# Kernel optimization log

Hardware: AMD Instinct MI355X
Metric: run time of the kernel (lower is better)

## Reference

```python
import jax, jax.numpy as jnp
import numpy as np

B, N, D, NS, HID = 256, 1024, 64, 8, 128
ITERS, SINK_ITERS, MESH_ITERS = 3, 8, 4
MESH_LR = 3.0
EPS = 1e-8


def _grid():
    # build_coords with latent_resolution=(32,32): meshgrid('xy'), flattened to [1024,2]
    x = np.linspace(0.0, 1.0, 32)
    xv, yv = np.meshgrid(x, x)
    g = np.stack([xv.reshape(-1), yv.reshape(-1)], axis=-1)
    return jnp.asarray(g, dtype=jnp.float32)


def layer_norm(x, g, b):
    m = jnp.mean(x, axis=-1, keepdims=True)
    v = jnp.var(x, axis=-1, keepdims=True)
    return (x - m) * jax.lax.rsqrt(v + 1e-5) * g + b


def cdist(k, q):
    # Euclidean pairwise distance: k [b,n,d], q [b,s,d] -> [b,n,s]
    d2 = (jnp.sum(k * k, -1)[..., :, None] + jnp.sum(q * q, -1)[..., None, :]
          - 2.0 * jnp.einsum('bnd,bsd->bns', k, q))
    return jnp.sqrt(jnp.maximum(d2, 1e-12))


def sinkhorn(C, a, b, u=None, v=None, n_iters=SINK_ITERS):
    # log-domain Sinkhorn; C [b,n,s], row marginal a [b,n], col marginal b [b,s]
    log_a = jnp.log(a + EPS)
    log_b = jnp.log(b + EPS)
    if u is None:
        u = jnp.zeros_like(a)
    if v is None:
        v = jnp.zeros_like(b)
    K = -C

    def body(carry, _):
        u, v = carry
        u = log_a - jax.scipy.special.logsumexp(K + v[..., None, :], axis=-1)
        v = log_b - jax.scipy.special.logsumexp(K + u[..., :, None], axis=-2)
        return (u, v), None

    (u, v), _ = jax.lax.scan(body, (u, v), None, length=n_iters)
    P = jnp.exp(K + u[..., :, None] + v[..., None, :])
    return P, u, v


def minimize_entropy_of_sinkhorn(C0, a, b, mesh_lr=MESH_LR, n_mesh_iters=MESH_ITERS):
    # MESH: gradient descent on the cost matrix to minimize Sinkhorn plan entropy
    def ent(C):
        P, u, v = sinkhorn(C, a, b)
        H = -jnp.sum(P * jnp.log(P + EPS))
        return H, (u, v)

    C = C0
    u = v = None
    for _ in range(n_mesh_iters):
        (_, (u, v)), g = jax.value_and_grad(ent, has_aux=True)(C)
        C = C - mesh_lr * g
    return C, u, v


def gru_cell(x, h, w_ih, w_hh, b_ih, b_hh):
    gi = x @ w_ih.T + b_ih
    gh = h @ w_hh.T + b_hh
    i_r, i_z, i_n = jnp.split(gi, 3, axis=-1)
    h_r, h_z, h_n = jnp.split(gh, 3, axis=-1)
    r = jax.nn.sigmoid(i_r + h_r)
    z = jax.nn.sigmoid(i_z + h_z)
    n = jnp.tanh(i_n + r * h_n)
    return (1.0 - z) * n + z * h


def setup_inputs() -> dict:
    key = jax.random.key(0)
    ks = jax.random.split(key, 16)
    s = D ** -0.5
    inp = {
        'inputs': jax.random.normal(ks[0], (B, N, D), jnp.float32),
        'noise': jax.random.normal(ks[1], (B, NS, D), jnp.float32),
        'slots_mu': jax.random.normal(ks[2], (1, 1, D), jnp.float32),
        'slots_sigma': jax.random.uniform(ks[3], (1, 1, D), jnp.float32),
        'Wq': jax.random.normal(ks[4], (D, D), jnp.float32) * s,
        'Wk': jax.random.normal(ks[5], (D, D), jnp.float32) * s,
        'Wv': jax.random.normal(ks[6], (D, D), jnp.float32) * s,
        'gru_w_ih': jax.random.normal(ks[7], (3 * D, D), jnp.float32) * s,
        'gru_w_hh': jax.random.normal(ks[8], (3 * D, D), jnp.float32) * s,
        'gru_b_ih': jnp.zeros((3 * D,), jnp.float32),
        'gru_b_hh': jnp.zeros((3 * D,), jnp.float32),
        'fc1_w': jax.random.normal(ks[9], (HID, D), jnp.float32) * s,
        'fc1_b': jnp.zeros((HID,), jnp.float32),
        'fc2_w': jax.random.normal(ks[10], (D, HID), jnp.float32) * (HID ** -0.5),
        'fc2_b': jnp.zeros((D,), jnp.float32),
        'ln_in_g': jnp.ones((D,), jnp.float32), 'ln_in_b': jnp.zeros((D,), jnp.float32),
        'ln_slots_g': jnp.ones((D,), jnp.float32), 'ln_slots_b': jnp.zeros((D,), jnp.float32),
        'ln_ff_g': jnp.ones((D,), jnp.float32), 'ln_ff_b': jnp.zeros((D,), jnp.float32),
        'wi_w': jax.random.normal(ks[11], (1, D), jnp.float32) * s,
        'wi_b': jnp.zeros((1,), jnp.float32),
        'ws_w': jax.random.normal(ks[12], (1, D), jnp.float32) * s,
        'ws_b': jnp.zeros((1,), jnp.float32),
    }
    return inp


def _forward(inputs, noise, slots_mu, slots_sigma, Wq, Wk, Wv,
             gru_w_ih, gru_w_hh, gru_b_ih, gru_b_hh,
             fc1_w, fc1_b, fc2_w, fc2_b,
             ln_in_g, ln_in_b, ln_slots_g, ln_slots_b, ln_ff_g, ln_ff_b,
             wi_w, wi_b, ws_w, ws_b):
    b_s, n, d = inputs.shape
    n_s = NS
    # slots ~ Normal(mu, |sigma|+eps) via reparameterized noise
    slots = slots_mu + (jnp.abs(slots_sigma) + EPS) * noise  # [b, n_s, d]

    x = layer_norm(inputs, ln_in_g, ln_in_b)
    k = x @ Wk.T
    v = x @ Wv.T
    grid = _grid()  # [N, 2]
    a = jax.nn.softmax((x @ wi_w.T + wi_b)[..., 0], axis=-1) * n_s  # [b, n]

    for _ in range(ITERS):
        slots_prev = slots
        s_n = layer_norm(slots, ln_slots_g, ln_slots_b)
        bm = jax.nn.softmax((s_n @ ws_w.T + ws_b)[..., 0], axis=-1) * n_s  # [b, n_s]
        q = s_n @ Wq.T
        C = cdist(k, q)  # [b, n, n_s]
        C, p, qq = minimize_entropy_of_sinkhorn(C, a, bm)
        attn, _, _ = sinkhorn(C, a, bm, u=p, v=qq)
        attn = jnp.transpose(attn, (0, 2, 1))  # [b, n_s, n]
        updates = attn @ v  # [b, n_s, d]
        slot_pos = jnp.einsum('bqk,kd->bqd', attn, grid)  # [b, n_s, 2]
        slots = gru_cell(updates.reshape(b_s * n_s, d),
                         slots_prev.reshape(b_s * n_s, d),
                         gru_w_ih, gru_w_hh, gru_b_ih, gru_b_hh).reshape(b_s, n_s, d)
        slots = slots + (jax.nn.relu(layer_norm(slots, ln_ff_g, ln_ff_b) @ fc1_w.T + fc1_b) @ fc2_w.T + fc2_b)
    return slots, slot_pos.reshape(b_s, n_s, 2), attn


def reference(inputs, noise, slots_mu, slots_sigma, Wq, Wk, Wv,
              gru_w_ih, gru_w_hh, gru_b_ih, gru_b_hh,
              fc1_w, fc1_b, fc2_w, fc2_b,
              ln_in_g, ln_in_b, ln_slots_g, ln_slots_b, ln_ff_g, ln_ff_b,
              wi_w, wi_b, ws_w, ws_b):
    return _forward(inputs, noise, slots_mu, slots_sigma, Wq, Wk, Wv,
                    gru_w_ih, gru_w_hh, gru_b_ih, gru_b_hh,
                    fc1_w, fc1_b, fc2_w, fc2_b,
                    ln_in_g, ln_in_b, ln_slots_g, ln_slots_b, ln_ff_g, ln_ff_b,
                    wi_w, wi_b, ws_w, ws_b)
```

## Files before the change

kernel.cpp:

```cpp
#include <hip/hip_runtime.h>
#include <math.h>

#define NB   256
#define NN   1024
#define ND   64
#define NSL  8
#define NHID 128
#define N_SINK 8
#define N_MESH 4
#define F_LR  3.0f
#define F_EPS 1e-8f

__global__ __launch_bounds__(256) void k_pre(
    const float* __restrict__ inp, const float* __restrict__ Wk,
    const float* __restrict__ lng, const float* __restrict__ lnb,
    const float* __restrict__ wiw, const float* __restrict__ wib,
    float* __restrict__ xout, float* __restrict__ kkout, float* __restrict__ wilog) {
  __shared__ __align__(16) float xs[4][64];
  int wv = threadIdx.x >> 6, ln = threadIdx.x & 63;
  size_t row = (size_t)blockIdx.x * 4 + wv;
  float xi = inp[row * 64 + ln];
  float s1 = xi, s2 = xi * xi;
  #pragma unroll
  for (int m = 32; m >= 1; m >>= 1) { s1 += __shfl_xor(s1, m, 64); s2 += __shfl_xor(s2, m, 64); }
  float mean = s1 * (1.f / 64.f);
  float var  = s2 * (1.f / 64.f) - mean * mean;
  float xn = (xi - mean) * rsqrtf(var + 1e-5f) * lng[ln] + lnb[ln];
  xs[wv][ln] = xn;
  xout[row * 64 + ln] = xn;
  float wl = xn * wiw[ln];
  #pragma unroll
  for (int m = 32; m >= 1; m >>= 1) wl += __shfl_xor(wl, m, 64);
  __syncthreads();
  const float4* w4 = (const float4*)(Wk + ln * 64);
  const float4* x4 = (const float4*)xs[wv];
  float ko = 0.f;
  #pragma unroll
  for (int c = 0; c < 16; ++c) {
    float4 a = w4[c], xv = x4[c];
    ko += a.x * xv.x + a.y * xv.y + a.z * xv.z + a.w * xv.w;
  }
  float kk = ko * ko;
  #pragma unroll
  for (int m = 32; m >= 1; m >>= 1) kk += __shfl_xor(kk, m, 64);
  if (ln == 0) { kkout[row] = kk; wilog[row] = wl + wib[0]; }
}

__global__ __launch_bounds__(1024) void k_mega(
    const float* __restrict__ noise, const float* __restrict__ mu,
    const float* __restrict__ sigma,
    const float* __restrict__ xg, const float* __restrict__ kkg,
    const float* __restrict__ wilogg,
    const float* __restrict__ Wq, const float* __restrict__ Wk,
    const float* __restrict__ Wv,
    const float* __restrict__ wih, const float* __restrict__ whh,
    const float* __restrict__ bih, const float* __restrict__ bhh,
    const float* __restrict__ fc1w, const float* __restrict__ fc1b,
    const float* __restrict__ fc2w, const float* __restrict__ fc2b,
    const float* __restrict__ lns_g, const float* __restrict__ lns_b,
    const float* __restrict__ lnf_g, const float* __restrict__ lnf_b,
    const float* __restrict__ wsw, const float* __restrict__ wsb,
    float* __restrict__ out_slots, float* __restrict__ out_pos,
    float* __restrict__ out_attn) {
  __shared__ __align__(16) float know[8][NN];
  __shared__ __align__(16) union {
    float fhist[N_SINK][NN];
    float part[16][8][64];
  } U;
  __shared__ __align__(16) float dsb[NN];
  __shared__ __align__(16) float slot_lds[8][64];
  __shared__ __align__(16) float sn[8][64];
  __shared__ __align__(16) float qsh[8][64];
  __shared__ __align__(16) float qs[8][64];
  __shared__ __align__(16) float updl[8][64];
  __shared__ __align__(16) float ys[8][64];
  __shared__ __align__(16) float rs[8][128];
  __shared__ float gbc[8];
  __shared__ float vbarbc[8];
  __shared__ float ghist[N_SINK][8];
  __shared__ float gBh[N_SINK][8];
  __shared__ float bmv[8], q2s[8], Bs[8], rBs[8];
  __shared__ float redf[16], bcf[1];

  int b = blockIdx.x, tid = threadIdx.x;
  int wv = tid >> 6, ln = tid & 63;

  if (tid < 512) {
    slot_lds[tid >> 6][ln] = mu[ln] + (fabsf(sigma[ln]) + F_EPS) * noise[(size_t)b * 512 + tid];
  }
  float wl = wilogg[(size_t)b * NN + tid];
  float m0 = wl;
  #pragma unroll
  for (int s = 32; s >= 1; s >>= 1) m0 = fmaxf(m0, __shfl_xor(m0, s, 64));
  if (ln == 0) redf[wv] = m0;
  __syncthreads();
  if (tid == 0) { float a = redf[0]; for (int w = 1; w < 16; ++w) a = fmaxf(a, redf[w]); bcf[0] = a; }
  __syncthreads();
  m0 = bcf[0];
  float e0 = __expf(wl - m0), se0 = e0;
  #pragma unroll
  for (int s = 32; s >= 1; s >>= 1) se0 += __shfl_xor(se0, s, 64);
  __syncthreads();
  if (ln == 0) redf[wv] = se0;
  __syncthreads();
  if (tid == 0) { float a = 0.f; for (int w = 0; w < 16; ++w) a += redf[w]; bcf[0] = a; }
  __syncthreads();
  float Ai  = 8.f * e0 / bcf[0] + F_EPS;
  float rAi = __frcp_rn(Ai);
  float kk = kkg[(size_t)b * NN + tid];
  const float4* xrow4 = (const float4*)(xg + ((size_t)b * NN + tid) * ND);

  for (int it = 0; it < 3; ++it) {
    if (wv < 8) {
      float x = slot_lds[wv][ln];
      float s1 = x, s2 = x * x;
      #pragma unroll
      for (int m = 32; m >= 1; m >>= 1) { s1 += __shfl_xor(s1, m, 64); s2 += __shfl_xor(s2, m, 64); }
      float mean = s1 * (1.f / 64.f);
      float var  = s2 * (1.f / 64.f) - mean * mean;
      float xn = (x - mean) * rsqrtf(var + 1e-5f) * lns_g[ln] + lns_b[ln];
      sn[wv][ln] = xn;
      float wlg = xn * wsw[ln];
      #pragma unroll
      for (int m = 32; m >= 1; m >>= 1) wlg += __shfl_xor(wlg, m, 64);
      if (ln == 0) bmv[wv] = wlg + wsb[0];
    }
    __syncthreads();
    if (wv < 8) {
      const float4* w4 = (const float4*)(Wq + ln * 64);
      const float4* x4 = (const float4*)sn[wv];
      float q = 0.f;
      #pragma unroll
      for (int c = 0; c < 16; ++c) {
        float4 a = w4[c], xv = x4[c];
        q += a.x * xv.x + a.y * xv.y + a.z * xv.z + a.w * xv.w;
      }
      qsh[wv][ln] = q;
      float q2 = q * q;
      #pragma unroll
      for (int m = 32; m >= 1; m >>= 1) q2 += __shfl_xor(q2, m, 64);
      if (ln == 0) q2s[wv] = q2;
    }
    if (tid >= 512 && tid < 520) {
      int j = tid - 512;
      float mx = bmv[0];
      #pragma unroll
      for (int jj = 1; jj < 8; ++jj) mx = fmaxf(mx, bmv[jj]);
      float ss = 0.f;
      #pragma unroll
      for (int jj = 0; jj < 8; ++jj) ss += __expf(bmv[jj] - mx);
      float Bj = 8.f * __expf(bmv[j] - mx) / ss + F_EPS;
      Bs[j] = Bj; rBs[j] = __frcp_rn(Bj);
    }
    __syncthreads();
    if (wv < 8) {
      float qt = 0.f;
      for (int o = 0; o < 64; ++o) qt = fmaf(qsh[wv][o], Wk[o * 64 + ln], qt);
      qs[wv][ln] = qt;
    }
    __syncthreads();

    float Mreg[8];
    {
      float dot[8];
      #pragma unroll
      for (int j = 0; j < 8; ++j) dot[j] = 0.f;
      #pragma unroll 4
      for (int c = 0; c < 16; ++c) {
        float4 xv = xrow4[c];
        #pragma unroll
        for (int j = 0; j < 8; ++j) {
          const float4 qv = *(const float4*)&qs[j][c * 4];
          dot[j] += xv.x * qv.x + xv.y * qv.y + xv.z * qv.z + xv.w * qv.w;
        }
      }
      #pragma unroll
      for (int j = 0; j < 8; ++j) {
        float d2 = kk + q2s[j] - 2.f * dot[j];
        float K = -sqrtf(fmaxf(d2, 1e-12f));
        Mreg[j] = __expf(K);
        know[j][tid] = Mreg[j];
      }
    }
    float f = 0.f;
    for (int phase = 0; phase <= N_MESH; ++phase) {
      bool cold = (phase < N_MESH);
      for (int t = 0; t < N_SINK; ++t) {
        float se = 0.f;
        if (cold && t == 0) {
          #pragma unroll
          for (int j = 0; j < 8; ++j) se += Mreg[j];
        } else {
          #pragma unroll
          for (int j = 0; j < 8; ++j) se += Mreg[j] * gbc[j];
        }
        f = __fdividef(Ai, se);
        U.fhist[t][tid] = f;
        __syncthreads();
        if (wv < 8) {
          float S = 0.f;
          #pragma unroll
          for (int k = 0; k < 16; ++k) {
            int i = ln + k * 64;
            S += know[wv][i] * U.fhist[t][i];
          }
          #pragma unroll
          for (int d = 32; d >= 1; d >>= 1) S += __shfl_xor(S, d, 64);
          if (ln == 0) {
            float g = __fdividef(Bs[wv], S);
            gbc[wv] = g; ghist[t][wv] = g; gBh[t][wv] = g * rBs[wv];
          }
        }
        __syncthreads();
      }
      if (phase == N_MESH) break;

      float Kbar[8], ubarT;
      {
        float gsum = 0.f;
        #pragma unroll
        for (int j = 0; j < 8; ++j) {
          float P  = Mreg[j] * f * gbc[j];
          float pe = P + F_EPS;
          float gp = -(__logf(pe) + __fdividef(P, pe)) * P;
          Kbar[j] = gp; gsum += gp;
        }
        ubarT = gsum;
      }
      if (wv < 8) {
        float gw = gbc[wv];
        float S = 0.f;
        #pragma unroll
        for (int k = 0; k < 16; ++k) {
          int i = ln + k * 64;
          float P  = know[wv][i] * U.fhist[N_SINK - 1][i] * gw;
          float pe = P + F_EPS;
          S += -(__logf(pe) + __fdividef(P, pe)) * P;
        }
        #pragma unroll
        for (int d = 32; d >= 1; d >>= 1) S += __shfl_xor(S, d, 64);
        if (ln == 0) vbarbc[wv] = S;
      }
      __syncthreads();
      for (int t = N_SINK - 1; t >= 0; --t) {
        float ft = U.fhist[t][tid];
        float dsum = (t == N_SINK - 1) ? ubarT : 0.f;
        #pragma unroll
        for (int j = 0; j < 8; ++j) {
          float vw = vbarbc[j] * gBh[t][j] * (Mreg[j] * ft);
          Kbar[j] -= vw; dsum -= vw;
        }
        float dfa = dsum * ft * rAi;
        if (t > 0) {
          #pragma unroll
          for (int j = 0; j < 8; ++j) Kbar[j] -= dfa * Mreg[j] * ghist[t - 1][j];
          dsb[tid] = dfa;
          __syncthreads();
          if (wv < 8) {
            float S = 0.f;
            #pragma unroll
            for (int k = 0; k < 16; ++k) {
              int i = ln + k * 64;
              S += know[wv][i] * dsb[i];
            }
            #pragma unroll
            for (int d = 32; d >= 1; d >>= 1) S += __shfl_xor(S, d, 64);
            if (ln == 0) vbarbc[wv] = -ghist[t - 1][wv] * S;
          }
          __syncthreads();
        } else {
          #pragma unroll
          for (int j = 0; j < 8; ++j) Kbar[j] -= dfa * Mreg[j];
        }
      }
      #pragma unroll
      for (int j = 0; j < 8; ++j) {
        Mreg[j] *= __expf(-F_LR * Kbar[j]);
        know[j][tid] = Mreg[j];
      }
    }
    #pragma unroll
    for (int j = 0; j < 8; ++j) {
      float P = Mreg[j] * f * gbc[j];
      know[j][tid] = P;
      if (it == 2) out_attn[((size_t)b * 8 + j) * NN + tid] = P;
    }
    __syncthreads();

    {
      float acc[8];
      #pragma unroll
      for (int j = 0; j < 8; ++j) acc[j] = 0.f;
      const float* xc = xg + ((size_t)b * NN + wv * 64) * ND + ln;
      #pragma unroll 2
      for (int i0 = 0; i0 < 64; i0 += 4) {
        float x0 = xc[(size_t)(i0 + 0) * 64];
        float x1 = xc[(size_t)(i0 + 1) * 64];
        float x2 = xc[(size_t)(i0 + 2) * 64];
        float x3 = xc[(size_t)(i0 + 3) * 64];
        int ir = wv * 64 + i0;
        #pragma unroll
        for (int j = 0; j < 8; ++j) {
          float4 a = *(const float4*)&know[j][ir];
          acc[j] += a.x * x0 + a.y * x1 + a.z * x2 + a.w * x3;
        }
      }
      #pragma unroll
      for (int j = 0; j < 8; ++j) U.part[wv][j][ln] = acc[j];
    }
    if (it == 2 && wv < 8) {
      float px = 0.f, py = 0.f;
      #pragma unroll
      for (int k = 0; k < 16; ++k) {
        int i = ln + k * 64;
        float a = know[wv][i];
        px += a * (float)(i & 31);
        py += a * (float)(i >> 5);
      }
      #pragma unroll
      for (int m = 32; m >= 1; m >>= 1) { px += __shfl_xor(px, m, 64); py += __shfl_xor(py, m, 64); }
      if (ln == 0) {
        out_pos[(b * 8 + wv) * 2 + 0] = px * (1.f / 31.f);
        out_pos[(b * 8 + wv) * 2 + 1] = py * (1.f / 31.f);
      }
    }
    __syncthreads();
    if (wv < 8) {
      float s = 0.f;
      #pragma unroll
      for (int w = 0; w < 16; ++w) s += U.part[w][wv][ln];
      updl[wv][ln] = s;
    }
    __syncthreads();
    if (wv < 8) {
      const float4* w4 = (const float4*)(Wv + ln * 64);
      const float4* u4 = (const float4*)updl[wv];
      float updv = 0.f;
      #pragma unroll
      for (int c = 0; c < 16; ++c) {
        float4 uv = u4[c], wvv = w4[c];
        updv += uv.x * wvv.x + uv.y * wvv.y + uv.z * wvv.z + uv.w * wvv.w;
      }
      sn[wv][ln] = updv;
    }
    __syncthreads();

    float hn = 0.f;
    if (wv < 8) {
      float h = slot_lds[wv][ln];
      float gi0 = bih[ln], gi1 = bih[64 + ln], gi2 = bih[128 + ln];
      float gh0 = bhh[ln], gh1 = bhh[64 + ln], gh2 = bhh[128 + ln];
      const float4* x4 = (const float4*)sn[wv];
      const float4* h4 = (const float4*)slot_lds[wv];
      const float4* wi0 = (const float4*)(wih + (size_t)ln * 64);
      const float4* wi1 = (const float4*)(wih + (size_t)(64 + ln) * 64);
      const float4* wi2 = (const float4*)(wih + (size_t)(128 + ln) * 64);
      const float4* wh0 = (const float4*)(whh + (size_t)ln * 64);
      const float4* wh1 = (const float4*)(whh + (size_t)(64 + ln) * 64);
      const float4* wh2 = (const float4*)(whh + (size_t)(128 + ln) * 64);
      #pragma unroll 2
      for (int c = 0; c < 16; ++c) {
        float4 xv = x4[c], hv = h4[c], a;
        a = wi0[c]; gi0 += xv.x * a.x + xv.y * a.y + xv.z * a.z + xv.w * a.w;
        a = wi1[c]; gi1 += xv.x * a.x + xv.y * a.y + xv.z * a.z + xv.w * a.w;
        a = wi2[c]; gi2 += xv.x * a.x + xv.y * a.y + xv.z * a.z + xv.w * a.w;
        a = wh0[c]; gh0 += hv.x * a.x + hv.y * a.y + hv.z * a.z + hv.w * a.w;
        a = wh1[c]; gh1 += hv.x * a.x + hv.y * a.y + hv.z * a.z + hv.w * a.w;
        a = wh2[c]; gh2 += hv.x * a.x + hv.y * a.y + hv.z * a.z + hv.w * a.w;
      }
      float r = 1.f / (1.f + expf(-(gi0 + gh0)));
      float z = 1.f / (1.f + expf(-(gi1 + gh1)));
      float n = tanhf(gi2 + r * gh2);
      hn = (1.f - z) * n + z * h;
      float s1 = hn, s2 = hn * hn;
      #pragma unroll
      for (int m = 32; m >= 1; m >>= 1) { s1 += __shfl_xor(s1, m, 64); s2 += __shfl_xor(s2, m, 64); }
      float mean = s1 * (1.f / 64.f);
      float var  = s2 * (1.f / 64.f) - mean * mean;
      ys[wv][ln] = (hn - mean) * rsqrtf(var + 1e-5f) * lnf_g[ln] + lnf_b[ln];
    }
    __syncthreads();
    if (wv < 8) {
      float a0 = fc1b[ln], a1 = fc1b[64 + ln];
      const float4* y4 = (const float4*)ys[wv];
      const float4* f0 = (const float4*)(fc1w + (size_t)ln * 64);
      const float4* f1 = (const float4*)(fc1w + (size_t)(64 + ln) * 64);
      #pragma unroll 2
      for (int c = 0; c < 16; ++c) {
        float4 yv = y4[c], a = f0[c], bb = f1[c];
        a0 += yv.x * a.x + yv.y * a.y + yv.z * a.z + yv.w * a.w;
        a1 += yv.x * bb.x + yv.y * bb.y + yv.z * bb.z + yv.w * bb.w;
      }
      rs[wv][ln] = fmaxf(a0, 0.f);
      rs[wv][64 + ln] = fmaxf(a1, 0.f);
    }
    __syncthreads();
    if (wv < 8) {
      float o = fc2b[ln];
      const float4* r4 = (const float4*)rs[wv];
      const float4* f2 = (const float4*)(fc2w + (size_t)ln * 128);
      #pragma unroll 2
      for (int c = 0; c < 32; ++c) {
        float4 rv = r4[c], a = f2[c];
        o += rv.x * a.x + rv.y * a.y + rv.z * a.z + rv.w * a.w;
      }
      slot_lds[wv][ln] = hn + o;
    }
    __syncthreads();
  }
  if (tid < 512) out_slots[(size_t)b * 512 + tid] = slot_lds[tid >> 6][ln];
}

extern "C" void kernel_launch(void* const* d_in, const int* in_sizes, int n_in,
                              void* d_out, int out_size, void* d_ws, size_t ws_size,
                              hipStream_t stream) {
  const float* inputs = (const float*)d_in[0];
  const float* noise  = (const float*)d_in[1];
  const float* mu     = (const float*)d_in[2];
  const float* sigma  = (const float*)d_in[3];
  const float* Wq     = (const float*)d_in[4];
  const float* Wk     = (const float*)d_in[5];
  const float* Wv     = (const float*)d_in[6];
  const float* gwih   = (const float*)d_in[7];
  const float* gwhh   = (const float*)d_in[8];
  const float* gbih   = (const float*)d_in[9];
  const float* gbhh   = (const float*)d_in[10];
  const float* fc1w   = (const float*)d_in[11];
  const float* fc1b   = (const float*)d_in[12];
  const float* fc2w   = (const float*)d_in[13];
  const float* fc2b   = (const float*)d_in[14];
  const float* lnin_g = (const float*)d_in[15];
  const float* lnin_b = (const float*)d_in[16];
  const float* lns_g  = (const float*)d_in[17];
  const float* lns_b  = (const float*)d_in[18];
  const float* lnf_g  = (const float*)d_in[19];
  const float* lnf_b  = (const float*)d_in[20];
  const float* wi_w   = (const float*)d_in[21];
  const float* wi_b   = (const float*)d_in[22];
  const float* ws_w   = (const float*)d_in[23];
  const float* ws_b   = (const float*)d_in[24];

  float* out       = (float*)d_out;
  float* out_slots = out;
  float* out_pos   = out + NB * NSL * ND;
  float* out_attn  = out_pos + NB * NSL * 2;

  float* p = (float*)d_ws;
  float* xbuf  = p; p += (size_t)NB * NN * ND;
  float* kkbuf = p; p += (size_t)NB * NN;
  float* wilog = p; p += (size_t)NB * NN;

  k_pre<<<(NB * NN) / 4, 256, 0, stream>>>(inputs, Wk, lnin_g, lnin_b, wi_w, wi_b,
                                           xbuf, kkbuf, wilog);
  k_mega<<<NB, 1024, 0, stream>>>(noise, mu, sigma, xbuf, kkbuf, wilog,
                                  Wq, Wk, Wv, gwih, gwhh, gbih, gbhh,
                                  fc1w, fc1b, fc2w, fc2b,
                                  lns_g, lns_b, lnf_g, lnf_b, ws_w, ws_b,
                                  out_slots, out_pos, out_attn);
}
```

Before: 1.109 ms.

## Replace LDS column reductions with register wave reductions and fewer barriers

```diff
diff --git a/kernel.cpp b/kernel.cpp
--- a/kernel.cpp
+++ b/kernel.cpp
@@ -44,6 +44,14 @@
   #pragma unroll
   for (int m = 32; m >= 1; m >>= 1) kk += __shfl_xor(kk, m, 64);
   if (ln == 0) { kkout[row] = kk; wilog[row] = wl + wib[0]; }
+}
+
+__device__ __forceinline__ void wave_sum8(float* a) {
+  #pragma unroll
+  for (int m = 32; m >= 1; m >>= 1) {
+    #pragma unroll
+    for (int j = 0; j < 8; ++j) a[j] += __shfl_xor(a[j], m, 64);
+  }
 }
 
 __global__ __launch_bounds__(1024) void k_mega(
@@ -67,7 +75,7 @@
     float fhist[N_SINK][NN];
     float part[16][8][64];
   } U;
-  __shared__ __align__(16) float dsb[NN];
+  __shared__ __align__(16) float part8[2][16][8];
   __shared__ __align__(16) float slot_lds[8][64];
   __shared__ __align__(16) float sn[8][64];
   __shared__ __align__(16) float qsh[8][64];
@@ -75,8 +83,6 @@
   __shared__ __align__(16) float updl[8][64];
   __shared__ __align__(16) float ys[8][64];
   __shared__ __align__(16) float rs[8][128];
-  __shared__ float gbc[8];
-  __shared__ float vbarbc[8];
   __shared__ float ghist[N_SINK][8];
   __shared__ float gBh[N_SINK][8];
   __shared__ float bmv[8], q2s[8], Bs[8], rBs[8];
@@ -160,6 +166,8 @@
     }
     __syncthreads();
 
+    float Bsr = 0.f, rBsr = 0.f;
+    if (ln < 8) { Bsr = Bs[ln]; rBsr = rBs[ln]; }
     float Mreg[8];
     {
       float dot[8];
@@ -177,12 +185,10 @@
       #pragma unroll
       for (int j = 0; j < 8; ++j) {
         float d2 = kk + q2s[j] - 2.f * dot[j];
-        float K = -sqrtf(fmaxf(d2, 1e-12f));
-        Mreg[j] = __expf(K);
-        know[j][tid] = Mreg[j];
-      }
-    }
-    float f = 0.f;
+        Mreg[j] = __expf(-sqrtf(fmaxf(d2, 1e-12f)));
+      }
+    }
+    float f = 0.f, g[8];
     for (int phase = 0; phase <= N_MESH; ++phase) {
       bool cold = (phase < N_MESH);
       for (int t = 0; t < N_SINK; ++t) {
@@ -192,96 +198,102 @@
           for (int j = 0; j < 8; ++j) se += Mreg[j];
         } else {
           #pragma unroll
-          for (int j = 0; j < 8; ++j) se += Mreg[j] * gbc[j];
+          for (int j = 0; j < 8; ++j) se += Mreg[j] * g[j];
         }
         f = __fdividef(Ai, se);
         U.fhist[t][tid] = f;
+        float pp[8];
+        #pragma unroll
+        for (int j = 0; j < 8; ++j) pp[j] = Mreg[j] * f;
+        wave_sum8(pp);
+        if (ln == 0) {
+          #pragma unroll
+          for (int j = 0; j < 8; ++j) part8[t & 1][wv][j] = pp[j];
+        }
         __syncthreads();
-        if (wv < 8) {
+        float gv = 0.f;
+        if (ln < 8) {
           float S = 0.f;
           #pragma unroll
-          for (int k = 0; k < 16; ++k) {
-            int i = ln + k * 64;
-            S += know[wv][i] * U.fhist[t][i];
-          }
-          #pragma unroll
-          for (int d = 32; d >= 1; d >>= 1) S += __shfl_xor(S, d, 64);
-          if (ln == 0) {
-            float g = __fdividef(Bs[wv], S);
-            gbc[wv] = g; ghist[t][wv] = g; gBh[t][wv] = g * rBs[wv];
-          }
-        }
-        __syncthreads();
+          for (int w = 0; w < 16; ++w) S += part8[t & 1][w][ln];
+          gv = __fdividef(Bsr, S);
+          if (wv == 0) { ghist[t][ln] = gv; gBh[t][ln] = gv * rBsr; }
+        }
+        #pragma unroll
+        for (int j = 0; j < 8; ++j) g[j] = __shfl(gv, j, 64);
       }
       if (phase == N_MESH) break;
 
-      float Kbar[8], ubarT;
+      float Kbar[8], vbar[8], ubarT;
       {
-        float gsum = 0.f;
+        float pp[8], gsum = 0.f;
         #pragma unroll
         for (int j = 0; j < 8; ++j) {
-          float P  = Mreg[j] * f * gbc[j];
+          float P  = Mreg[j] * f * g[j];
           float pe = P + F_EPS;
           float gp = -(__logf(pe) + __fdividef(P, pe)) * P;
-          Kbar[j] = gp; gsum += gp;
+          Kbar[j] = gp; gsum += gp; pp[j] = gp;
         }
         ubarT = gsum;
-      }
-      if (wv < 8) {
-        float gw = gbc[wv];
-        float S = 0.f;
-        #pragma unroll
-        for (int k = 0; k < 16; ++k) {
-          int i = ln + k * 64;
-          float P  = know[wv][i] * U.fhist[N_SINK - 1][i] * gw;
-          float pe = P + F_EPS;
-          S += -(__logf(pe) + __fdividef(P, pe)) * P;
-        }
-        #pragma unroll
-        for (int d = 32; d >= 1; d >>= 1) S += __shfl_xor(S, d, 64);
-        if (ln == 0) vbarbc[wv] = S;
-      }
-      __syncthreads();
+        wave_sum8(pp);
+        if (ln == 0) {
+          #pragma unroll
+          for (int j = 0; j < 8; ++j) part8[0][wv][j] = pp[j];
+        }
+        __syncthreads();
+        float sv = 0.f;
+        if (ln < 8) {
+          float S = 0.f;
+          #pragma unroll
+          for (int w = 0; w < 16; ++w) S += part8[0][w][ln];
+          sv = S;
+        }
+        #pragma unroll
+        for (int j = 0; j < 8; ++j) vbar[j] = __shfl(sv, j, 64);
+      }
       for (int t = N_SINK - 1; t >= 0; --t) {
         float ft = U.fhist[t][tid];
         float dsum = (t == N_SINK - 1) ? ubarT : 0.f;
         #pragma unroll
         for (int j = 0; j < 8; ++j) {
-          float vw = vbarbc[j] * gBh[t][j] * (Mreg[j] * ft);
+          float vw = vbar[j] * gBh[t][j] * (Mreg[j] * ft);
           Kbar[j] -= vw; dsum -= vw;
         }
         float dfa = dsum * ft * rAi;
         if (t > 0) {
-          #pragma unroll
-          for (int j = 0; j < 8; ++j) Kbar[j] -= dfa * Mreg[j] * ghist[t - 1][j];
-          dsb[tid] = dfa;
+          float pp[8];
+          #pragma unroll
+          for (int j = 0; j < 8; ++j) {
+            float gm = ghist[t - 1][j];
+            Kbar[j] -= dfa * Mreg[j] * gm;
+            pp[j] = Mreg[j] * dfa;
+          }
+          wave_sum8(pp);
+          if (ln == 0) {
+            #pragma unroll
+            for (int j = 0; j < 8; ++j) part8[t & 1][wv][j] = pp[j];
+          }
           __syncthreads();
-          if (wv < 8) {
+          float sv = 0.f;
+          if (ln < 8) {
             float S = 0.f;
             #pragma unroll
-            for (int k = 0; k < 16; ++k) {
-              int i = ln + k * 64;
-              S += know[wv][i] * dsb[i];
-            }
-            #pragma unroll
-            for (int d = 32; d >= 1; d >>= 1) S += __shfl_xor(S, d, 64);
-            if (ln == 0) vbarbc[wv] = -ghist[t - 1][wv] * S;
+            for (int w = 0; w < 16; ++w) S += part8[t & 1][w][ln];
+            sv = -ghist[t - 1][ln] * S;
           }
-          __syncthreads();
+          #pragma unroll
+          for (int j = 0; j < 8; ++j) vbar[j] = __shfl(sv, j, 64);
         } else {
           #pragma unroll
           for (int j = 0; j < 8; ++j) Kbar[j] -= dfa * Mreg[j];
         }
       }
       #pragma unroll
-      for (int j = 0; j < 8; ++j) {
-        Mreg[j] *= __expf(-F_LR * Kbar[j]);
-        know[j][tid] = Mreg[j];
-      }
+      for (int j = 0; j < 8; ++j) Mreg[j] *= __expf(-F_LR * Kbar[j]);
     }
     #pragma unroll
     for (int j = 0; j < 8; ++j) {
-      float P = Mreg[j] * f * gbc[j];
+      float P = Mreg[j] * f * g[j];
       know[j][tid] = P;
       if (it == 2) out_attn[((size_t)b * 8 + j) * NN + tid] = P;
     }
```

After: 1.525 ms. 1.37x slower.
